# Performance work log

Measured on AMD Instinct MI355X. Metric: run time of the kernel, lower is better.

## Reference

```python
import jax, jax.numpy as jnp
import numpy as np

N = 50000      # nodes
E = 800000     # edges
IN = 64        # in_channels
HID = 128      # hidden_channels
HEADS = 4
D = HID // HEADS  # 32 per-head dim
G = 64         # graphs in batch


def setup_inputs() -> dict:
    key = jax.random.key(0)
    ks = jax.random.split(key, 24)
    def p(k, shape):
        return (jax.random.normal(k, shape, jnp.float32) * 0.05)
    x = jax.random.normal(ks[0], (N, IN), jnp.float32)
    edge_index = jax.random.randint(ks[1], (2, E), 0, N, dtype=jnp.int32).astype(jnp.int64)
    batch = jnp.sort(jax.random.randint(ks[2], (N,), 0, G, dtype=jnp.int32)).astype(jnp.int64)
    inp = {"x": x, "edge_index": edge_index, "batch": batch}
    # layer 1: in -> HID (heads*D), with root/skip projection
    inp["Wq1"] = p(ks[3], (IN, HID)); inp["bq1"] = p(ks[4], (HID,))
    inp["Wk1"] = p(ks[5], (IN, HID)); inp["bk1"] = p(ks[6], (HID,))
    inp["Wv1"] = p(ks[7], (IN, HID)); inp["bv1"] = p(ks[8], (HID,))
    inp["Ws1"] = p(ks[9], (IN, HID)); inp["bs1"] = p(ks[10], (HID,))
    # layer 2: HID -> HID
    inp["Wq2"] = p(ks[11], (HID, HID)); inp["bq2"] = p(ks[12], (HID,))
    inp["Wk2"] = p(ks[13], (HID, HID)); inp["bk2"] = p(ks[14], (HID,))
    inp["Wv2"] = p(ks[15], (HID, HID)); inp["bv2"] = p(ks[16], (HID,))
    inp["Ws2"] = p(ks[17], (HID, HID)); inp["bs2"] = p(ks[18], (HID,))
    # readout linear HID -> 2
    inp["Wl"] = p(ks[19], (HID, 2)); inp["bl"] = p(ks[20], (2,))
    return inp


def transformer_conv(x, src, dst, Wq, bq, Wk, bk, Wv, bv, Ws, bs):
    """PyG TransformerConv (concat=True, root_weight=True, beta=False, eval mode)."""
    n = x.shape[0]
    q = (x @ Wq + bq).reshape(n, HEADS, D)
    k = (x @ Wk + bk).reshape(n, HEADS, D)
    v = (x @ Wv + bv).reshape(n, HEADS, D)
    # per-edge attention logits: query at target (dst), key/value at source (src)
    qi, kj, vj = q[dst], k[src], v[src]           # [E, H, D]
    logits = jnp.sum(qi * kj, axis=-1) / jnp.sqrt(jnp.asarray(D, x.dtype))  # [E, H]
    # segment softmax over incoming edges of each target node
    m = jax.ops.segment_max(logits, dst, num_segments=n)   # [N, H]
    p = jnp.exp(logits - m[dst])                           # [E, H]
    s = jax.ops.segment_sum(p, dst, num_segments=n)        # [N, H]
    alpha = p / s[dst]                                     # [E, H]
    agg = jax.ops.segment_sum(alpha[..., None] * vj, dst, num_segments=n)  # [N, H, D]
    out = agg.reshape(n, HID) + (x @ Ws + bs)              # concat heads + skip
    return out


def reference(x, edge_index, batch,
              Wq1, bq1, Wk1, bk1, Wv1, bv1, Ws1, bs1,
              Wq2, bq2, Wk2, bk2, Wv2, bv2, Ws2, bs2,
              Wl, bl):
    src, dst = edge_index[0], edge_index[1]
    h = jax.nn.relu(transformer_conv(x, src, dst, Wq1, bq1, Wk1, bk1, Wv1, bv1, Ws1, bs1))
    h = jax.nn.relu(transformer_conv(h, src, dst, Wq2, bq2, Wk2, bk2, Wv2, bv2, Ws2, bs2))
    # global mean pool per graph
    counts = jax.ops.segment_sum(jnp.ones((h.shape[0],), h.dtype), batch, num_segments=G)
    pooled = jax.ops.segment_sum(h, batch, num_segments=G) / jnp.maximum(counts, 1.0)[:, None]
    return pooled @ Wl + bl  # [G, 2]
```

## Files before the change

### kernel.cpp

```cpp
#include <hip/hip_runtime.h>
#include <hip/hip_bf16.h>
#include <cstdint>
#include <cstddef>

#define N_NODES 50000
#define N_EDGES 800000
#define IN_CH 64
#define HID_CH 128
#define N_GRAPHS 64

#define NB_SCAN ((N_NODES + 255) / 256)
#define NB_CNT  ((N_EDGES + 255) / 256)
#define NB_GEMM ((N_NODES + 63) / 64)
#define W_ELEMS (4 * IN_CH * 128 + 4 * HID_CH * 128)
#define NB_CONV ((W_ELEMS + 255) / 256)

typedef short s16x8 __attribute__((ext_vector_type(8)));
typedef float f32x4 __attribute__((ext_vector_type(4)));
typedef float f32x2 __attribute__((ext_vector_type(2)));

__device__ __forceinline__ float bf2f(__hip_bfloat16 v) { return __bfloat162float(v); }
__device__ __forceinline__ float bfbits2f(unsigned hs) {
  union { unsigned u; float f; } v; v.u = hs << 16; return v.f;
}
__device__ __forceinline__ float bfhi2f(unsigned w) {
  union { unsigned u; float f; } v; v.u = w & 0xffff0000u; return v.f;
}
__device__ __forceinline__ short f2bfs(float f) {
  __hip_bfloat16 h = __float2bfloat16(f); return *(short*)&h;
}
__device__ __forceinline__ unsigned short f2bfu(float f) {
  __hip_bfloat16 h = __float2bfloat16(f); return *(unsigned short*)&h;
}
__device__ __forceinline__ int clamp_id(int v) {
  if (v < 0) v = 0;
  if (v >= N_NODES) v = N_NODES - 1;
  return v;
}

__device__ __forceinline__ unsigned char f2fp8(float v) {
  return (unsigned char)(__builtin_amdgcn_cvt_pk_fp8_f32(v, v, 0, false) & 0xff);
}
template<bool HI>
__device__ __forceinline__ f32x2 fp8pair(unsigned w) {
  return __builtin_amdgcn_cvt_pk_f32_fp8(w, HI);
}

__global__ __launch_bounds__(256)
void prep(const float* __restrict__ w1q, const float* __restrict__ w1k,
          const float* __restrict__ w1v, const float* __restrict__ w1s,
          const float* __restrict__ w2q, const float* __restrict__ w2k,
          const float* __restrict__ w2v, const float* __restrict__ w2s,
          __hip_bfloat16* d1q, __hip_bfloat16* d1k, __hip_bfloat16* d1v, __hip_bfloat16* d1s,
          __hip_bfloat16* d2q, __hip_bfloat16* d2k, __hip_bfloat16* d2v, __hip_bfloat16* d2s,
          int* cnt, int* tmp, float* pooled)
{
  int bx = blockIdx.x;
  if (bx < NB_SCAN) {
    int i = bx * 256 + threadIdx.x;
    if (i < N_NODES) { cnt[i] = 0; tmp[i] = 0; }
    if (i < N_GRAPHS * HID_CH) pooled[i] = 0.f;
    return;
  }
  int j = (bx - NB_SCAN) * 256 + threadIdx.x;
  if (j >= W_ELEMS) return;
  const float* S[8] = {w1q, w1k, w1v, w1s, w2q, w2k, w2v, w2s};
  __hip_bfloat16* D[8] = {d1q, d1k, d1v, d1s, d2q, d2k, d2v, d2s};
  int m, r;
  if (j < 4 * IN_CH * 128) { m = j >> 13; r = j & 8191; }
  else { int jj = j - 4 * IN_CH * 128; m = 4 + (jj >> 14); r = jj & 16383; }
  int k = r >> 7, c = r & 127;
  D[m][(((k >> 3) * 128 + c) << 3) + (k & 7)] = __float2bfloat16(S[m][r]);
}

__global__ void count_deg(const int* __restrict__ ei, int* __restrict__ cnt) {
  int e = blockIdx.x * blockDim.x + threadIdx.x;
  if (e < N_EDGES) atomicAdd(&cnt[clamp_id(ei[N_EDGES + e])], 1);
}

template<int KD, int XF32>
__device__ __forceinline__ void gemm_body(
    int bg, const void* X,
    const short* __restrict__ WTq, const short* __restrict__ WTk,
    const short* __restrict__ WTv, const short* __restrict__ WTs,
    const float* __restrict__ bq, const float* __restrict__ bk,
    const float* __restrict__ bv, const float* __restrict__ bs,
    short* Qo, unsigned char* KV8, short* So, short* lds)
{
  constexpr int KT = KD / 32;
  constexpr int CHUNKS = KD * 16;
  const int tid  = threadIdx.x;
  const int wid  = tid >> 6;
  const int lane = tid & 63;
  const int quad = lane >> 4;
  const int mm   = lane & 15;
  const int rt   = wid & 1;
  const int ch   = wid >> 1;
  const int rowbase = bg * 64 + rt * 32;

  s16x8 afrag[2][KT];
  #pragma unroll
  for (int t = 0; t < 2; ++t) {
    const int arow = rowbase + t * 16 + mm;
    if (arow < N_NODES) {
      if (XF32) {
        const float* xp = (const float*)X + (size_t)arow * KD;
        #pragma unroll
        for (int kt = 0; kt < KT; ++kt) {
          const float4* p = (const float4*)(xp + kt * 32 + quad * 8);
          float4 a = p[0], b = p[1];
          s16x8 fr;
          fr[0] = f2bfs(a.x); fr[1] = f2bfs(a.y); fr[2] = f2bfs(a.z); fr[3] = f2bfs(a.w);
          fr[4] = f2bfs(b.x); fr[5] = f2bfs(b.y); fr[6] = f2bfs(b.z); fr[7] = f2bfs(b.w);
          afrag[t][kt] = fr;
        }
      } else {
        const short* xp = (const short*)X + (size_t)arow * KD;
        #pragma unroll
        for (int kt = 0; kt < KT; ++kt)
          afrag[t][kt] = *(const s16x8*)(xp + kt * 32 + quad * 8);
      }
    } else {
      #pragma unroll
      for (int kt = 0; kt < KT; ++kt)
        afrag[t][kt] = (s16x8){0,0,0,0,0,0,0,0};
    }
  }

  const short* wts[4] = {WTq, WTk, WTv, WTs};
  const float* bias[4] = {bq, bk, bv, bs};

  #pragma unroll
  for (int mat = 0; mat < 4; ++mat) {
    if (mat > 0) __syncthreads();
    {
      const uint4* src = (const uint4*)wts[mat];
      uint4* dst = (uint4*)lds;
      #pragma unroll
      for (int i = 0; i < CHUNKS / 256; ++i)
        dst[tid + i * 256] = src[tid + i * 256];
    }
    __syncthreads();

    f32x4 acc[4][2];
    #pragma unroll
    for (int c4 = 0; c4 < 4; ++c4) {
      float b = bias[mat][ch * 64 + c4 * 16 + mm];
      f32x4 av = {b, b, b, b};
      acc[c4][0] = av; acc[c4][1] = av;
    }
    #pragma unroll
    for (int kt = 0; kt < KT; ++kt) {
      #pragma unroll
      for (int c4 = 0; c4 < 4; ++c4) {
        s16x8 bfrag = *(const s16x8*)(lds + ((((kt * 4 + quad) << 7) + ch * 64 + c4 * 16 + mm) << 3));
        acc[c4][0] = __builtin_amdgcn_mfma_f32_16x16x32_bf16(afrag[0][kt], bfrag, acc[c4][0], 0, 0, 0);
        acc[c4][1] = __builtin_amdgcn_mfma_f32_16x16x32_bf16(afrag[1][kt], bfrag, acc[c4][1], 0, 0, 0);
      }
    }
    if (mat == 1 || mat == 2) {
      unsigned char* O8 = KV8 + ((mat == 1) ? 0 : 128);
      #pragma unroll
      for (int c4 = 0; c4 < 4; ++c4) {
        const int col = ch * 64 + c4 * 16 + mm;
        #pragma unroll
        for (int t = 0; t < 2; ++t) {
          #pragma unroll
          for (int r = 0; r < 4; ++r) {
            int row = rowbase + t * 16 + quad * 4 + r;
            if (row < N_NODES)
              O8[(size_t)row * 256 + col] = f2fp8(acc[c4][t][r]);
          }
        }
      }
    } else {
      short* O = (mat == 0) ? Qo : So;
      #pragma unroll
      for (int c4 = 0; c4 < 4; ++c4) {
        const int col = ch * 64 + c4 * 16 + mm;
        #pragma unroll
        for (int t = 0; t < 2; ++t) {
          #pragma unroll
          for (int r = 0; r < 4; ++r) {
            int row = rowbase + t * 16 + quad * 4 + r;
            if (row < N_NODES)
              ((__hip_bfloat16*)O)[(size_t)row * 128 + col] = __float2bfloat16(acc[c4][t][r]);
          }
        }
      }
    }
  }
}

__global__ __launch_bounds__(256)
void scan1(const int* __restrict__ cnt, int* __restrict__ offs, int* __restrict__ bsum) {
  __shared__ int wsum[4];
  int t = threadIdx.x, lane = t & 63, w = t >> 6;
  int i = blockIdx.x * 256 + t;
  int v = (i < N_NODES) ? cnt[i] : 0;
  int x = v;
  #pragma unroll
  for (int o = 1; o < 64; o <<= 1) { int y = __shfl_up(x, o, 64); if (lane >= o) x += y; }
  if (lane == 63) wsum[w] = x;
  __syncthreads();
  if (t == 0) {
    int run = 0;
    #pragma unroll
    for (int k = 0; k < 4; ++k) { int tv = wsum[k]; wsum[k] = run; run += tv; }
    bsum[blockIdx.x] = run;
  }
  __syncthreads();
  if (i <= N_NODES) offs[i] = wsum[w] + x - v;
}

__global__ __launch_bounds__(256)
void scan2(int* __restrict__ bsum) {
  __shared__ int wsum[4];
  int t = threadIdx.x, lane = t & 63, w = t >> 6;
  int v = (t < NB_SCAN) ? bsum[t] : 0;
  int x = v;
  #pragma unroll
  for (int o = 1; o < 64; o <<= 1) { int y = __shfl_up(x, o, 64); if (lane >= o) x += y; }
  if (lane == 63) wsum[w] = x;
  __syncthreads();
  if (t == 0) {
    int run = 0;
    #pragma unroll
    for (int k = 0; k < 4; ++k) { int tv = wsum[k]; wsum[k] = run; run += tv; }
  }
  __syncthreads();
  if (t < NB_SCAN) bsum[t] = wsum[w] + x - v;
}

__global__ __launch_bounds__(256)
void scatter_gemm1(const int* __restrict__ ei, const int* __restrict__ offs,
                   const int* __restrict__ bsum, int* __restrict__ tmp, int* __restrict__ ssrc,
                   const float* __restrict__ X,
                   const short* __restrict__ w1q, const short* __restrict__ w1k,
                   const short* __restrict__ w1v, const short* __restrict__ w1s,
                   const float* __restrict__ b1q, const float* __restrict__ b1k,
                   const float* __restrict__ b1v, const float* __restrict__ b1s,
                   short* Qb, unsigned char* KV8, short* Sb)
{
  __shared__ short lds[IN_CH * 128];
  int bx = blockIdx.x;
  if (bx >= NB_GEMM) {
    int e = (bx - NB_GEMM) * 256 + threadIdx.x;
    if (e < N_EDGES) {
      int src = clamp_id(ei[e]);
      int dst = clamp_id(ei[N_EDGES + e]);
      int pos = offs[dst] + bsum[dst >> 8] + atomicAdd(&tmp[dst], 1);
      ssrc[pos] = src;
    }
    return;
  }
  gemm_body<IN_CH, 1>(bx, X, w1q, w1k, w1v, w1s, b1q, b1k, b1v, b1s,
                      Qb, KV8, Sb, lds);
}

__global__ __launch_bounds__(256)
void attn_kernel(const unsigned short* __restrict__ Q, const unsigned char* __restrict__ KV8,
                 const unsigned short* S,
                 const int* __restrict__ offs, const int* __restrict__ bsum,
                 const int* __restrict__ ssrc, unsigned short* H)
{
  const int dst = blockIdx.x * 4 + (threadIdx.x >> 6);
  if (dst >= N_NODES) return;
  const int lane = threadIdx.x & 63;
  const int sub  = lane >> 4;
  const int cl   = lane & 15;

  const float qs = 0.17677669529663687f * 1.4426950408889634f;
  uint4 qw = *(const uint4*)(Q + (size_t)dst * 128 + cl * 8);
  float q[8], a[8];
  #pragma unroll
  for (int i = 0; i < 4; ++i) {
    unsigned w = ((unsigned*)&qw)[i];
    q[2 * i]     = bfbits2f(w & 0xffffu) * qs;
    q[2 * i + 1] = bfhi2f(w) * qs;
    a[2 * i] = 0.f; a[2 * i + 1] = 0.f;
  }
  float s = 0.f;

  const int e0 = offs[dst] + bsum[dst >> 8];
  const int e1 = offs[dst + 1] + bsum[(dst + 1) >> 8];
  const int iters = (e1 - e0 + 3) >> 2;

  if (iters > 0) {
    int e = e0 + sub;
    bool have = (e < e1);
    int src = have ? ssrc[e] : ssrc[e0];
    float ph = have ? 1.f : 0.f;
    const unsigned char* kvp = KV8 + (size_t)src * 256 + cl * 8;
    uint2 kw = *(const uint2*)(kvp);
    uint2 vw = *(const uint2*)(kvp + 128);

    for (int it = 0; it < iters; ++it) {
      uint2 kwn, vwn;
      int en = e + 4;
      bool haven = (en < e1);
      float phn = haven ? 1.f : 0.f;
      if (it + 1 < iters) {
        int srcn = haven ? ssrc[en] : ssrc[e0];
        const unsigned char* kvn = KV8 + (size_t)srcn * 256 + cl * 8;
        kwn = *(const uint2*)(kvn);
        vwn = *(const uint2*)(kvn + 128);
      } else {
        kwn = kw; vwn = vw;
      }
      f32x2 k0 = fp8pair<false>(kw.x), k1 = fp8pair<true>(kw.x);
      f32x2 k2 = fp8pair<false>(kw.y), k3 = fp8pair<true>(kw.y);
      float d = q[0] * k0.x + q[1] * k0.y + q[2] * k1.x + q[3] * k1.y
              + q[4] * k2.x + q[5] * k2.y + q[6] * k3.x + q[7] * k3.y;
      d += __shfl_xor(d, 1, 64);
      d += __shfl_xor(d, 2, 64);
      float p = exp2f(d) * ph;
      s += p;
      f32x2 v0 = fp8pair<false>(vw.x), v1 = fp8pair<true>(vw.x);
      f32x2 v2 = fp8pair<false>(vw.y), v3 = fp8pair<true>(vw.y);
      a[0] += p * v0.x; a[1] += p * v0.y;
      a[2] += p * v1.x; a[3] += p * v1.y;
      a[4] += p * v2.x; a[5] += p * v2.y;
      a[6] += p * v3.x; a[7] += p * v3.y;
      kw = kwn; vw = vwn; ph = phn; e = en;
    }
  }

  s += __shfl_xor(s, 16, 64);
  s += __shfl_xor(s, 32, 64);
  #pragma unroll
  for (int i = 0; i < 8; ++i) {
    a[i] += __shfl_xor(a[i], 16, 64);
    a[i] += __shfl_xor(a[i], 32, 64);
  }
  const float inv = (s > 0.f) ? (1.0f / s) : 0.f;

  if (sub == 0) {
    uint4 sw = *(const uint4*)(S + (size_t)dst * 128 + cl * 8);
    uint4 ow;
    #pragma unroll
    for (int i = 0; i < 4; ++i) {
      unsigned w = ((unsigned*)&sw)[i];
      float o0 = fmaxf(a[2 * i] * inv     + bfbits2f(w & 0xffffu), 0.f);
      float o1 = fmaxf(a[2 * i + 1] * inv + bfhi2f(w), 0.f);
      ((unsigned*)&ow)[i] = (unsigned)f2bfu(o0) | ((unsigned)f2bfu(o1) << 16);
    }
    *(uint4*)(H + (size_t)dst * 128 + cl * 8) = ow;
  }
}

__global__ __launch_bounds__(256)
void gemm2(const short* __restrict__ X,
           const short* __restrict__ w2q, const short* __restrict__ w2k,
           const short* __restrict__ w2v, const short* __restrict__ w2s,
           const float* __restrict__ b2q, const float* __restrict__ b2k,
           const float* __restrict__ b2v, const float* __restrict__ b2s,
           short* Qb, unsigned char* KV8, short* Sb)
{
  __shared__ short lds[HID_CH * 128];
  gemm_body<HID_CH, 0>(blockIdx.x, X, w2q, w2k, w2v, w2s, b2q, b2k, b2v, b2s,
                       Qb, KV8, Sb, lds);
}

__device__ __forceinline__ int lower_bound_i(const int* __restrict__ b, int n, int val) {
  int lo = 0, hi = n;
  while (lo < hi) { int mid = (lo + hi) >> 1; if (b[mid] < val) lo = mid + 1; else hi = mid; }
  return lo;
}

__global__ __launch_bounds__(128)
void pool_partial(const __hip_bfloat16* __restrict__ H, const int* __restrict__ batch,
                  float* __restrict__ pooled)
{
  const int g = blockIdx.x >> 4, p = blockIdx.x & 15, t = threadIdx.x;
  const int s = lower_bound_i(batch, N_NODES, g);
  const int e = lower_bound_i(batch, N_NODES, g + 1);
  const int len = e - s;
  if (len <= 0) return;
  const int chunk = (len + 15) >> 4;
  const int a = s + p * chunk;
  const int b = min(a + chunk, e);
  if (a >= b) return;
  float sum = 0.f;
  for (int i = a; i < b; ++i) sum += bf2f(H[(size_t)i * 128 + t]);
  atomicAdd(&pooled[g * 128 + t], sum);
}

__global__ __launch_bounds__(128)
void pool_final(const float* __restrict__ pooled, const int* __restrict__ batch,
                const float* __restrict__ Wl, const float* __restrict__ bl,
                float* __restrict__ out)
{
  const int g = blockIdx.x, t = threadIdx.x;
  __shared__ float r0[128], r1[128];
  const int s = lower_bound_i(batch, N_NODES, g);
  const int e = lower_bound_i(batch, N_NODES, g + 1);
  const float inv = 1.0f / (float)max(e - s, 1);
  const float pc = pooled[g * 128 + t] * inv;
  r0[t] = pc * Wl[t * 2 + 0];
  r1[t] = pc * Wl[t * 2 + 1];
  __syncthreads();
  for (int o = 64; o > 0; o >>= 1) {
    if (t < o) { r0[t] += r0[t + o]; r1[t] += r1[t + o]; }
    __syncthreads();
  }
  if (t == 0) {
    out[g * 2 + 0] = r0[0] + bl[0];
    out[g * 2 + 1] = r1[0] + bl[1];
  }
}


extern "C" void kernel_launch(void* const* d_in, const int* in_sizes, int n_in,
                              void* d_out, int out_size, void* d_ws, size_t ws_size,
                              hipStream_t stream) {
  uintptr_t base = (uintptr_t)d_ws;
  auto take = [&](size_t bytes) -> uintptr_t {
    uintptr_t p = base;
    base += (bytes + 255) & ~(size_t)255;
    return p;
  };

  int*   cnt    = (int*)take((size_t)N_NODES * 4);
  int*   tmp    = (int*)take((size_t)N_NODES * 4);
  int*   offs   = (int*)take((size_t)(N_NODES + 1) * 4);
  int*   bsum   = (int*)take((size_t)NB_SCAN * 4);
  int*   ssrc   = (int*)take((size_t)N_EDGES * 4);
  short* Qb     = (short*)take((size_t)N_NODES * 128 * 2);
  unsigned char* KV8 = (unsigned char*)take((size_t)N_NODES * 256);
  short* Sb     = (short*)take((size_t)N_NODES * 128 * 2);
  short* wt1q   = (short*)take((size_t)IN_CH * 128 * 2);
  short* wt1k   = (short*)take((size_t)IN_CH * 128 * 2);
  short* wt1v   = (short*)take((size_t)IN_CH * 128 * 2);
  short* wt1s   = (short*)take((size_t)IN_CH * 128 * 2);
  short* wt2q   = (short*)take((size_t)HID_CH * 128 * 2);
  short* wt2k   = (short*)take((size_t)HID_CH * 128 * 2);
  short* wt2v   = (short*)take((size_t)HID_CH * 128 * 2);
  short* wt2s   = (short*)take((size_t)HID_CH * 128 * 2);
  float* pooled = (float*)take((size_t)N_GRAPHS * 128 * 4);

  const int* ei    = (const int*)d_in[1];
  const int* batch = (const int*)d_in[2];

  prep<<<NB_SCAN + NB_CONV, 256, 0, stream>>>(
      (const float*)d_in[3], (const float*)d_in[5], (const float*)d_in[7], (const float*)d_in[9],
      (const float*)d_in[11], (const float*)d_in[13], (const float*)d_in[15], (const float*)d_in[17],
      (__hip_bfloat16*)wt1q, (__hip_bfloat16*)wt1k, (__hip_bfloat16*)wt1v, (__hip_bfloat16*)wt1s,
      (__hip_bfloat16*)wt2q, (__hip_bfloat16*)wt2k, (__hip_bfloat16*)wt2v, (__hip_bfloat16*)wt2s,
      cnt, tmp, pooled);

  count_deg<<<NB_CNT, 256, 0, stream>>>(ei, cnt);

  scan1<<<NB_SCAN, 256, 0, stream>>>(cnt, offs, bsum);
  scan2<<<1, 256, 0, stream>>>(bsum);

  scatter_gemm1<<<NB_GEMM + NB_CNT, 256, 0, stream>>>(
      ei, offs, bsum, tmp, ssrc,
      (const float*)d_in[0],
      wt1q, wt1k, wt1v, wt1s,
      (const float*)d_in[4], (const float*)d_in[6], (const float*)d_in[8], (const float*)d_in[10],
      Qb, KV8, Sb);

  const int attn_grid = (N_NODES + 3) / 4;

  attn_kernel<<<attn_grid, 256, 0, stream>>>(
      (const unsigned short*)Qb, KV8,
      (const unsigned short*)Sb, offs, bsum, ssrc, (unsigned short*)Sb);

  gemm2<<<NB_GEMM, 256, 0, stream>>>(
      Sb, wt2q, wt2k, wt2v, wt2s,
      (const float*)d_in[12], (const float*)d_in[14], (const float*)d_in[16], (const float*)d_in[18],
      Qb, KV8, Sb);

  attn_kernel<<<attn_grid, 256, 0, stream>>>(
      (const unsigned short*)Qb, KV8,
      (const unsigned short*)Sb, offs, bsum, ssrc, (unsigned short*)Sb);

  pool_partial<<<N_GRAPHS * 16, 128, 0, stream>>>(
      (const __hip_bfloat16*)Sb, batch, pooled);
  pool_final<<<N_GRAPHS, 128, 0, stream>>>(pooled, batch, (const float*)d_in[19],
                                           (const float*)d_in[20], (float*)d_out);
}
```

Baseline: 314.1 us.

## Record per-edge rank during degree count to drop second atomic pass in CSR build

The degree-count atomics now run inside the prep kernel and save each edge's returned slot (rank) as a 16-bit value. The scatter phase then places edges at offs+bsum+rank without a second round of atomics on a tmp counter. Zeroing moves to a single memset over a contiguous workspace span, and both the count and scatter phases handle four edges per thread with vector loads. This adds a 1.6 MB rank array and a memset launch, and it assumes no node has an in-degree above 65535.

```diff
diff --git a/kernel.cpp b/kernel.cpp
--- a/kernel.cpp
+++ b/kernel.cpp
@@ -10,7 +10,7 @@
 #define N_GRAPHS 64
 
 #define NB_SCAN ((N_NODES + 255) / 256)
-#define NB_CNT  ((N_EDGES + 255) / 256)
+#define NB_CNT4 ((N_EDGES + 1023) / 1024)
 #define NB_GEMM ((N_NODES + 63) / 64)
 #define W_ELEMS (4 * IN_CH * 128 + 4 * HID_CH * 128)
 #define NB_CONV ((W_ELEMS + 255) / 256)
@@ -47,22 +47,35 @@
 }
 
 __global__ __launch_bounds__(256)
-void prep(const float* __restrict__ w1q, const float* __restrict__ w1k,
+void prep(const int* __restrict__ ei, int* __restrict__ cnt,
+          unsigned short* __restrict__ rank,
+          const float* __restrict__ w1q, const float* __restrict__ w1k,
           const float* __restrict__ w1v, const float* __restrict__ w1s,
           const float* __restrict__ w2q, const float* __restrict__ w2k,
           const float* __restrict__ w2v, const float* __restrict__ w2s,
           __hip_bfloat16* d1q, __hip_bfloat16* d1k, __hip_bfloat16* d1v, __hip_bfloat16* d1s,
-          __hip_bfloat16* d2q, __hip_bfloat16* d2k, __hip_bfloat16* d2v, __hip_bfloat16* d2s,
-          int* cnt, int* tmp, float* pooled)
+          __hip_bfloat16* d2q, __hip_bfloat16* d2k, __hip_bfloat16* d2v, __hip_bfloat16* d2s)
 {
   int bx = blockIdx.x;
-  if (bx < NB_SCAN) {
-    int i = bx * 256 + threadIdx.x;
-    if (i < N_NODES) { cnt[i] = 0; tmp[i] = 0; }
-    if (i < N_GRAPHS * HID_CH) pooled[i] = 0.f;
+  if (bx < NB_CNT4) {
+    int e0 = bx * 1024 + threadIdx.x * 4;
+    if (e0 >= N_EDGES) return;
+    if (e0 + 3 < N_EDGES) {
+      int4 dv = *(const int4*)(ei + N_EDGES + e0);
+      unsigned short r0 = (unsigned short)atomicAdd(&cnt[clamp_id(dv.x)], 1);
+      unsigned short r1 = (unsigned short)atomicAdd(&cnt[clamp_id(dv.y)], 1);
+      unsigned short r2 = (unsigned short)atomicAdd(&cnt[clamp_id(dv.z)], 1);
+      unsigned short r3 = (unsigned short)atomicAdd(&cnt[clamp_id(dv.w)], 1);
+      ushort4 rv; rv.x = r0; rv.y = r1; rv.z = r2; rv.w = r3;
+      *(ushort4*)(rank + e0) = rv;
+    } else {
+      for (int j = 0; j < 4; ++j)
+        if (e0 + j < N_EDGES)
+          rank[e0 + j] = (unsigned short)atomicAdd(&cnt[clamp_id(ei[N_EDGES + e0 + j])], 1);
+    }
     return;
   }
-  int j = (bx - NB_SCAN) * 256 + threadIdx.x;
+  int j = (bx - NB_CNT4) * 256 + threadIdx.x;
   if (j >= W_ELEMS) return;
   const float* S[8] = {w1q, w1k, w1v, w1s, w2q, w2k, w2v, w2s};
   __hip_bfloat16* D[8] = {d1q, d1k, d1v, d1s, d2q, d2k, d2v, d2s};
@@ -71,11 +84,6 @@
   else { int jj = j - 4 * IN_CH * 128; m = 4 + (jj >> 14); r = jj & 16383; }
   int k = r >> 7, c = r & 127;
   D[m][(((k >> 3) * 128 + c) << 3) + (k & 7)] = __float2bfloat16(S[m][r]);
-}
-
-__global__ void count_deg(const int* __restrict__ ei, int* __restrict__ cnt) {
-  int e = blockIdx.x * blockDim.x + threadIdx.x;
-  if (e < N_EDGES) atomicAdd(&cnt[clamp_id(ei[N_EDGES + e])], 1);
 }
 
 template<int KD, int XF32>
@@ -234,7 +242,8 @@
 
 __global__ __launch_bounds__(256)
 void scatter_gemm1(const int* __restrict__ ei, const int* __restrict__ offs,
-                   const int* __restrict__ bsum, int* __restrict__ tmp, int* __restrict__ ssrc,
+                   const int* __restrict__ bsum, const unsigned short* __restrict__ rank,
+                   int* __restrict__ ssrc,
                    const float* __restrict__ X,
                    const short* __restrict__ w1q, const short* __restrict__ w1k,
                    const short* __restrict__ w1v, const short* __restrict__ w1s,
@@ -245,12 +254,31 @@
   __shared__ short lds[IN_CH * 128];
   int bx = blockIdx.x;
   if (bx >= NB_GEMM) {
-    int e = (bx - NB_GEMM) * 256 + threadIdx.x;
-    if (e < N_EDGES) {
-      int src = clamp_id(ei[e]);
-      int dst = clamp_id(ei[N_EDGES + e]);
-      int pos = offs[dst] + bsum[dst >> 8] + atomicAdd(&tmp[dst], 1);
-      ssrc[pos] = src;
+    int e0 = (bx - NB_GEMM) * 1024 + threadIdx.x * 4;
+    if (e0 >= N_EDGES) return;
+    if (e0 + 3 < N_EDGES) {
+      int4 sv = *(const int4*)(ei + e0);
+      int4 dv = *(const int4*)(ei + N_EDGES + e0);
+      ushort4 rv = *(const ushort4*)(rank + e0);
+      int d0 = clamp_id(dv.x), d1 = clamp_id(dv.y);
+      int d2 = clamp_id(dv.z), d3 = clamp_id(dv.w);
+      int p0 = offs[d0] + bsum[d0 >> 8] + rv.x;
+      int p1 = offs[d1] + bsum[d1 >> 8] + rv.y;
+      int p2 = offs[d2] + bsum[d2 >> 8] + rv.z;
+      int p3 = offs[d3] + bsum[d3 >> 8] + rv.w;
+      ssrc[p0] = clamp_id(sv.x);
+      ssrc[p1] = clamp_id(sv.y);
+      ssrc[p2] = clamp_id(sv.z);
+      ssrc[p3] = clamp_id(sv.w);
+    } else {
+      for (int j = 0; j < 4; ++j) {
+        int e = e0 + j;
+        if (e < N_EDGES) {
+          int src = clamp_id(ei[e]);
+          int dst = clamp_id(ei[N_EDGES + e]);
+          ssrc[offs[dst] + bsum[dst >> 8] + rank[e]] = src;
+        }
+      }
     }
     return;
   }
@@ -422,10 +450,11 @@
   };
 
   int*   cnt    = (int*)take((size_t)N_NODES * 4);
-  int*   tmp    = (int*)take((size_t)N_NODES * 4);
+  float* pooled = (float*)take((size_t)N_GRAPHS * 128 * 4);
   int*   offs   = (int*)take((size_t)(N_NODES + 1) * 4);
   int*   bsum   = (int*)take((size_t)NB_SCAN * 4);
   int*   ssrc   = (int*)take((size_t)N_EDGES * 4);
+  unsigned short* rank = (unsigned short*)take((size_t)N_EDGES * 2);
   short* Qb     = (short*)take((size_t)N_NODES * 128 * 2);
   unsigned char* KV8 = (unsigned char*)take((size_t)N_NODES * 256);
   short* Sb     = (short*)take((size_t)N_NODES * 128 * 2);
@@ -437,25 +466,25 @@
   short* wt2k   = (short*)take((size_t)HID_CH * 128 * 2);
   short* wt2v   = (short*)take((size_t)HID_CH * 128 * 2);
   short* wt2s   = (short*)take((size_t)HID_CH * 128 * 2);
-  float* pooled = (float*)take((size_t)N_GRAPHS * 128 * 4);
 
   const int* ei    = (const int*)d_in[1];
   const int* batch = (const int*)d_in[2];
 
-  prep<<<NB_SCAN + NB_CONV, 256, 0, stream>>>(
+  size_t zspan = (size_t)((char*)pooled + (size_t)N_GRAPHS * 128 * 4 - (char*)cnt);
+  hipMemsetAsync(cnt, 0, zspan, stream);
+
+  prep<<<NB_CNT4 + NB_CONV, 256, 0, stream>>>(
+      ei, cnt, rank,
       (const float*)d_in[3], (const float*)d_in[5], (const float*)d_in[7], (const float*)d_in[9],
       (const float*)d_in[11], (const float*)d_in[13], (const float*)d_in[15], (const float*)d_in[17],
       (__hip_bfloat16*)wt1q, (__hip_bfloat16*)wt1k, (__hip_bfloat16*)wt1v, (__hip_bfloat16*)wt1s,
-      (__hip_bfloat16*)wt2q, (__hip_bfloat16*)wt2k, (__hip_bfloat16*)wt2v, (__hip_bfloat16*)wt2s,
-      cnt, tmp, pooled);
-
-  count_deg<<<NB_CNT, 256, 0, stream>>>(ei, cnt);
+      (__hip_bfloat16*)wt2q, (__hip_bfloat16*)wt2k, (__hip_bfloat16*)wt2v, (__hip_bfloat16*)wt2s);
 
   scan1<<<NB_SCAN, 256, 0, stream>>>(cnt, offs, bsum);
   scan2<<<1, 256, 0, stream>>>(bsum);
 
-  scatter_gemm1<<<NB_GEMM + NB_CNT, 256, 0, stream>>>(
-      ei, offs, bsum, tmp, ssrc,
+  scatter_gemm1<<<NB_GEMM + NB_CNT4, 256, 0, stream>>>(
+      ei, offs, bsum, rank, ssrc,
       (const float*)d_in[0],
       wt1q, wt1k, wt1v, wt1s,
       (const float*)d_in[4], (const float*)d_in[6], (const float*)d_in[8], (const float*)d_in[10],
```

New measurement: 294.0 us. 1.07x faster.
